# Optimization experiments

Measured on AMD Instinct MI355X. Metric: run time of the kernel, lower is better.

## Reference

```python
import jax, jax.numpy as jnp
import numpy as np
from jax import lax

SOS = -1
BLANK = 28
MAX_SYMBOLS = 4
T, B, ENC = 128, 32, 1024
VOCAB = 29   # includes blank at index 28
EMB = 320
HID = 320


def setup_inputs() -> dict:
    key = jax.random.key(0)
    ks = jax.random.split(key, 9)
    s = 0.1
    return {
        "x": jax.random.normal(ks[0], (T, B, ENC), jnp.float32),
        "lengths": jax.random.randint(ks[1], (B,), T // 2, T + 1, jnp.int32),
        "embedding": jax.random.normal(ks[2], (VOCAB - 1, EMB), jnp.float32) * s,
        "W_ih": jax.random.normal(ks[3], (4 * HID, EMB), jnp.float32) * s,
        "W_hh": jax.random.normal(ks[4], (4 * HID, HID), jnp.float32) * s,
        "b_ih": jax.random.normal(ks[5], (4 * HID,), jnp.float32) * s,
        "b_hh": jax.random.normal(ks[6], (4 * HID,), jnp.float32) * s,
        "W_joint": jax.random.normal(ks[7], (VOCAB, ENC + HID), jnp.float32) * s,
        "b_joint": jax.random.normal(ks[8], (VOCAB,), jnp.float32) * s,
    }


def _lstm_cell(xe, h, c, W_ih, W_hh, b_ih, b_hh):
    gates = xe @ W_ih.T + h @ W_hh.T + b_ih + b_hh          # [B, 4H]
    i, f, g, o = jnp.split(gates, 4, axis=-1)               # torch gate order
    i, f, o = jax.nn.sigmoid(i), jax.nn.sigmoid(f), jax.nn.sigmoid(o)
    g = jnp.tanh(g)
    c2 = f * c + i * g
    h2 = o * jnp.tanh(c2)
    return h2, c2


def _decode(x, lengths, embedding, W_ih, W_hh, b_ih, b_hh, W_joint, b_joint):
    Tn, Bn, _ = x.shape
    Lmax = Tn * MAX_SYMBOLS
    bidx = jnp.arange(Bn)

    def sym_step(carry, _):
        h, c, last, pos, labels, lps, active = carry
        # pred step: zero embedding for SOS, else embed (label>blank -> label-1)
        adj = jnp.where(last > BLANK, last - 1, last)
        adj = jnp.clip(adj, 0, VOCAB - 2)
        emb = jnp.where((last == SOS)[:, None], 0.0, embedding[adj])  # [B, EMB]
        h2, c2 = _lstm_cell(emb, h, c, W_ih, W_hh, b_ih, b_hh)
        # joint step: concat(enc frame, pred) -> fc -> log_softmax
        f_enc = carry_f                                            # closed over
        logits = jnp.concatenate([f_enc, h2], axis=-1) @ W_joint.T + b_joint
        logp = jax.nn.log_softmax(logits, axis=-1)                 # [B, V]
        idx = jnp.argmax(logp, axis=-1).astype(jnp.int32)
        v = jnp.take_along_axis(logp, idx[:, None].astype(jnp.int32), axis=-1)[:, 0]
        is_blank = idx == BLANK
        emit = active & (~is_blank)
        # commit hidden/label only on non-blank emission (as original)
        h = jnp.where(emit[:, None], h2, h)
        c = jnp.where(emit[:, None], c2, c)
        last = jnp.where(emit, idx, last)
        cur = labels[bidx, pos]
        labels = labels.at[bidx, pos].set(jnp.where(emit, idx, cur))
        lps = lps + jnp.where(active, v, 0.0)
        pos = pos + emit.astype(pos.dtype)
        active = active & (~is_blank)
        return (h, c, last, pos, labels, lps, active), None

    def time_step(carry, inp):
        f_t, t = inp                                              # f_t: [B, ENC]
        h, c, last, pos, labels, lps = carry
        active0 = t < lengths
        global carry_f
        carry_f = f_t
        (h, c, last, pos, labels, lps, _), _ = lax.scan(
            sym_step, (h, c, last, pos, labels, lps, active0), None,
            length=MAX_SYMBOLS)
        return (h, c, last, pos, labels, lps), None

    init = (
        jnp.zeros((Bn, HID), x.dtype),
        jnp.zeros((Bn, HID), x.dtype),
        jnp.full((Bn,), SOS, jnp.int32),
        jnp.zeros((Bn,), jnp.int32),
        jnp.full((Bn, Lmax), -1, jnp.int32),
        jnp.zeros((Bn,), x.dtype),
    )
    (h, c, last, pos, labels, lps), _ = lax.scan(
        time_step, init, (x, jnp.arange(Tn)))
    return labels, pos, lps


def reference(x, lengths, embedding, W_ih, W_hh, b_ih, b_hh, W_joint, b_joint):
    # labels: [B, T*MAX_SYMBOLS] int32, padded with -1
    # n_symbols: [B] number of emitted symbols per utterance
    # logp_sum: [B] sum of selected max log-probs over all evaluated decode steps
    labels, n_symbols, logp_sum = _decode(
        x, lengths, embedding, W_ih, W_hh, b_ih, b_hh, W_joint, b_joint)
    return labels, n_symbols, logp_sum
```

## Files before the change

### kernel.cpp

```cpp
#include <hip/hip_runtime.h>
#include <math.h>

typedef unsigned long long u64;
typedef unsigned int u32;

#define BN 32
#define TN 128
#define ENCD 1024
#define HID 320
#define NG 1280
#define VN 29
#define BLANKI 28
#define SLICES 8
#define UPS 40
#define ROWS 160
#define JW 1344
#define JSTR 41
#define XSTRIDE 70
#define NPOLL (7*69)

#define E_OFF   0
#define E_SZ    (TN*BN*VN)
#define P_OFF   (E_OFF + E_SZ)
#define P_SZ    (VN*NG)
#define X_OFF   (P_OFF + P_SZ)
#define X_U64S  (2*BN*SLICES*XSTRIDE)

__device__ __forceinline__ float dot4(float4 a, float4 b) {
    return a.x*b.x + a.y*b.y + a.z*b.z + a.w*b.w;
}
__device__ __forceinline__ u64 aload(const u64* p) {
    return __hip_atomic_load(p, __ATOMIC_RELAXED, __HIP_MEMORY_SCOPE_AGENT);
}
__device__ __forceinline__ void astore(u64* p, u64 v) {
    __hip_atomic_store(p, v, __ATOMIC_RELAXED, __HIP_MEMORY_SCOPE_AGENT);
}

__global__ __launch_bounds__(256) void k_enc(const float* __restrict__ x,
        const float* __restrict__ Wj, const float* __restrict__ bj,
        float* __restrict__ E, u64* __restrict__ xchg)
{
    __shared__ float xl[4][1056];
    const int tid = threadIdx.x;
    const int blk = blockIdx.x;
    const int t = blk >> 3, b0 = (blk & 7) * 4;

    if (tid < 35) xchg[(size_t)blk*35 + tid] = 0ull;

    #pragma unroll
    for (int bb = 0; bb < 4; ++bb) {
        const float4* src = (const float4*)(x + ((size_t)(t*BN + b0 + bb))*ENCD);
        float4 v4 = src[tid];
        ((float4*)&xl[bb][0])[tid + (tid >> 5)] = v4;
    }
    __syncthreads();
    if (tid < 232) {
        const int v = tid >> 3, k8 = tid & 7;
        float a0=0.f, a1=0.f, a2=0.f, a3=0.f;
        const float4* wrow = (const float4*)(Wj + (size_t)v*JW) + k8*32;
        const float4* x0 = ((const float4*)&xl[0][0]) + k8*33;
        const float4* x1 = ((const float4*)&xl[1][0]) + k8*33;
        const float4* x2 = ((const float4*)&xl[2][0]) + k8*33;
        const float4* x3 = ((const float4*)&xl[3][0]) + k8*33;
        #pragma unroll 4
        for (int m = 0; m < 32; ++m) {
            float4 w4 = wrow[m];
            a0 += dot4(w4, x0[m]);
            a1 += dot4(w4, x1[m]);
            a2 += dot4(w4, x2[m]);
            a3 += dot4(w4, x3[m]);
        }
        #pragma unroll
        for (int d = 1; d < 8; d <<= 1) {
            a0 += __shfl_xor(a0, d); a1 += __shfl_xor(a1, d);
            a2 += __shfl_xor(a2, d); a3 += __shfl_xor(a3, d);
        }
        if (k8 == 0) {
            float bjv = bj[v];
            E[((size_t)(t*BN + b0+0))*VN + v] = a0 + bjv;
            E[((size_t)(t*BN + b0+1))*VN + v] = a1 + bjv;
            E[((size_t)(t*BN + b0+2))*VN + v] = a2 + bjv;
            E[((size_t)(t*BN + b0+3))*VN + v] = a3 + bjv;
        }
    }
}

__global__ __launch_bounds__(256) void k_pred(const float* __restrict__ emb,
        const float* __restrict__ Wih, const float* __restrict__ bih,
        const float* __restrict__ bhh, float* __restrict__ P)
{
    __shared__ float el[HID];
    const int tid = threadIdx.x, j = blockIdx.x;
    if (tid < 80) {
        float4 v4 = make_float4(0.f, 0.f, 0.f, 0.f);
        if (j < 28) v4 = ((const float4*)(emb + (size_t)j*HID))[tid];
        ((float4*)el)[tid] = v4;
    }
    __syncthreads();
    #pragma unroll
    for (int q = 0; q < 5; ++q) {
        const int r = q*256 + tid;
        float acc = bih[r] + bhh[r];
        const float4* wrow = (const float4*)(Wih + (size_t)r*HID);
        #pragma unroll 8
        for (int k4 = 0; k4 < 80; ++k4)
            acc += dot4(wrow[k4], ((const float4*)el)[k4]);
        P[(size_t)j*NG + r] = acc;
    }
}

__global__ __launch_bounds__(256, 1) void k_dec(const int* __restrict__ lengths,
        const float* __restrict__ Whh, const float* __restrict__ Wj,
        const float* __restrict__ E, const float* __restrict__ P,
        u64* __restrict__ xchg, float* __restrict__ out)
{
    __shared__ float P_lds[VN*ROWS];
    __shared__ float Wjh[VN*JSTR];
    __shared__ float h2st[HID];
    __shared__ float c2st[UPS];
    __shared__ float gates[ROWS];
    __shared__ float plog_l[SLICES*VN];
    __shared__ float pad_force[14400];

    const int tid = threadIdx.x;
    const int bid = blockIdx.x;
    const int b = bid & 31, slice = bid >> 5;
    const int rg = tid >> 3, kg = tid & 7;
    const int lane = tid & 63;

    int len = lengths[b];
    if (len > TN) len = TN;
    if (len < 0) {
        pad_force[tid] = (float)tid;
        gates[tid & 127] = pad_force[(tid*7) & 14399];
    }

    float4 wq[50];
    #pragma unroll
    for (int q = 0; q < 5; ++q) {
        const int r = rg*5 + q;
        const int gt = r / 40, u = r - gt*40;
        const float4* wrow = (const float4*)(Whh + ((size_t)(gt*HID + slice*UPS + u))*HID + kg*40);
        #pragma unroll
        for (int jb = 0; jb < 10; ++jb) wq[q*10 + jb] = wrow[jb];
    }
    for (int i = tid; i < VN*ROWS; i += 256) {
        const int jj = i / ROWS, r = i - jj*ROWS;
        const int gt = r / 40, u = r - gt*40;
        P_lds[i] = P[(size_t)jj*NG + gt*HID + slice*UPS + u];
    }
    for (int i = tid; i < VN*UPS; i += 256) {
        const int v = i / UPS, k = i - v*UPS;
        Wjh[v*JSTR + k] = Wj[(size_t)v*JW + ENCD + slice*UPS + k];
    }
    if (tid < UPS) c2st[tid] = 0.f;
    if (slice == 0) for (int i = tid; i < 512; i += 256) out[b*512 + i] = -1.0f;
    __syncthreads();

    float lps = 0.f;
    float acc[5] = {0.f, 0.f, 0.f, 0.f, 0.f};
    float lsum_r = 0.f;
    int pos = 0, jrow = 28, n = 1;
    bool dirty = true;

    const int pw1 = tid;
    const bool has2 = (tid < NPOLL - 256);

    for (int t = 0; t < len; ++t) {
        const float Ereg = (lane < VN)
            ? E[((size_t)(t*BN + b))*VN + lane] : -INFINITY;

        for (int s = 0; s < 4; ++s) {
            if (dirty) {
                const int par = n & 1;
                const size_t mybase = ((size_t)(par*BN + b)*SLICES + slice)*XSTRIDE;
                if (kg == 0) {
                    #pragma unroll
                    for (int q = 0; q < 5; ++q) {
                        const int r = rg*5 + q;
                        gates[r] = acc[q] + P_lds[jrow*ROWS + r];
                    }
                }
                __syncthreads();
                if (tid < 64) {
                    if (tid < UPS) {
                        const float gi = gates[tid],      gf = gates[40+tid];
                        const float gg = gates[80+tid],   go = gates[120+tid];
                        const float ii = 1.f/(1.f+expf(-gi));
                        const float ff = 1.f/(1.f+expf(-gf));
                        const float oo = 1.f/(1.f+expf(-go));
                        const float G  = tanhf(gg);
                        const float c2 = ff*c2st[tid] + ii*G;
                        c2st[tid] = c2;
                        const float h2 = oo * tanhf(c2);
                        h2st[slice*UPS + tid] = h2;
                        const u64 pk = ((u64)(u32)n << 32) | (u64)__float_as_uint(h2);
                        astore(&xchg[mybase + tid], pk);
                    }
                    if (tid < VN) {
                        float pkv[8];
                        #pragma unroll
                        for (int k8 = 0; k8 < 8; ++k8) {
                            float pk = 0.f;
                            #pragma unroll
                            for (int m2 = 0; m2 < 5; ++m2)
                                pk += Wjh[tid*JSTR + k8*5 + m2]
                                    * h2st[slice*UPS + k8*5 + m2];
                            pkv[k8] = pk;
                        }
                        const float pp = ((pkv[0]+pkv[1])+(pkv[2]+pkv[3]))
                                       + ((pkv[4]+pkv[5])+(pkv[6]+pkv[7]));
                        plog_l[slice*VN + tid] = pp;
                        const u64 pk2 = ((u64)(u32)n << 32) | (u64)__float_as_uint(pp);
                        astore(&xchg[mybase + UPS + tid], pk2);
                    }
                }
                {
                    const size_t pbase = ((size_t)(par*BN + b)*SLICES)*XSTRIDE;
                    int j1 = pw1 / 69; const int w1 = pw1 - j1*69;
                    j1 += (j1 >= slice);
                    u64* p1 = (u64*)&xchg[pbase + (size_t)j1*XSTRIDE + w1];
                    bool need1 = true, need2 = has2;
                    int j2 = 0, w2 = 0; u64* p2 = p1;
                    if (has2) {
                        const int i2 = tid + 256;
                        j2 = i2 / 69; w2 = i2 - j2*69;
                        j2 += (j2 >= slice);
                        p2 = (u64*)&xchg[pbase + (size_t)j2*XSTRIDE + w2];
                    }
                    int cap = 0;
                    while ((need1 | need2) && cap < (1 << 16)) {
                        u64 v1 = 0, v2 = 0;
                        if (need1) v1 = aload(p1);
                        if (need2) v2 = aload(p2);
                        if (need1 && (u32)(v1 >> 32) == (u32)n) {
                            const float f = __uint_as_float((u32)v1);
                            if (w1 < UPS) h2st[j1*UPS + w1] = f;
                            else          plog_l[j1*VN + (w1 - UPS)] = f;
                            need1 = false;
                        }
                        if (need2 && (u32)(v2 >> 32) == (u32)n) {
                            const float f = __uint_as_float((u32)v2);
                            if (w2 < UPS) h2st[j2*UPS + w2] = f;
                            else          plog_l[j2*VN + (w2 - UPS)] = f;
                            need2 = false;
                        }
                        ++cap;
                    }
                }
                __syncthreads();
                {
                    float a2[5] = {0.f, 0.f, 0.f, 0.f, 0.f};
                    #pragma unroll
                    for (int jb = 0; jb < 10; ++jb) {
                        float4 hv = *(const float4*)(h2st + kg*40 + jb*4);
                        #pragma unroll
                        for (int q = 0; q < 5; ++q) a2[q] += dot4(wq[q*10 + jb], hv);
                    }
                    #pragma unroll
                    for (int q = 0; q < 5; ++q) {
                        a2[q] += __shfl_xor(a2[q], 1);
                        a2[q] += __shfl_xor(a2[q], 2);
                        a2[q] += __shfl_xor(a2[q], 4);
                        acc[q] = a2[q];
                    }
                }
                if (lane < VN) {
                    float sA = 0.f;
                    #pragma unroll
                    for (int j2 = 0; j2 < SLICES; ++j2) sA += plog_l[j2*VN + lane];
                    lsum_r = sA;
                }
                n++;
            }
            const float Lv = (lane < VN) ? (Ereg + lsum_r) : -INFINITY;
            float m = Lv; int ai = lane;
            #pragma unroll
            for (int d = 1; d < 64; d <<= 1) {
                const float om = __shfl_xor(m, d);
                const int   oi = __shfl_xor(ai, d);
                if (om > m || (om == m && oi < ai)) { m = om; ai = oi; }
            }
            float e = (lane < VN) ? expf(Lv - m) : 0.f;
            #pragma unroll
            for (int d = 1; d < 64; d <<= 1) e += __shfl_xor(e, d);
            lps += -logf(e);

            if (ai == BLANKI) { dirty = false; break; }
            if (slice == 0 && tid == 0) out[b*512 + pos] = (float)ai;
            pos++;
            jrow = ai;
            dirty = true;
        }
    }

    if (slice == 0 && tid == 0) {
        out[16384 + b] = (float)pos;
        out[16416 + b] = lps;
    }
}

extern "C" void kernel_launch(void* const* d_in, const int* in_sizes, int n_in,
                              void* d_out, int out_size, void* d_ws, size_t ws_size,
                              hipStream_t stream) {
    const float* x    = (const float*)d_in[0];
    const int* lens   = (const int*)  d_in[1];
    const float* emb  = (const float*)d_in[2];
    const float* Wih  = (const float*)d_in[3];
    const float* Whh  = (const float*)d_in[4];
    const float* bih  = (const float*)d_in[5];
    const float* bhh  = (const float*)d_in[6];
    const float* Wj   = (const float*)d_in[7];
    const float* bj   = (const float*)d_in[8];
    float* out = (float*)d_out;
    float* ws  = (float*)d_ws;

    float* E    = ws + E_OFF;
    float* P    = ws + P_OFF;
    u64*   xchg = (u64*)(ws + X_OFF);

    hipLaunchKernelGGL(k_enc,  dim3(1024), dim3(256), 0, stream, x, Wj, bj, E, xchg);
    hipLaunchKernelGGL(k_pred, dim3(29),   dim3(256), 0, stream, emb, Wih, bih, bhh, P);
    hipLaunchKernelGGL(k_dec,  dim3(256),  dim3(256), 0, stream,
                       lens, Whh, Wj, E, P, xchg, out);
}
```

Measured before the change: 1.643 ms.

## Compute full joint pred projection locally instead of exchanging partial logits

Each decoder block stops publishing per-slice partial joint logits through the global exchange buffer. It now polls only the hidden-state slices of the other blocks and computes the full hidden-to-vocab projection locally, with the weights held in registers. This shrinks the exchange record per slice and removes the 29-element logit work from the critical path before publishing. Polling moves to threads 64 and up so the gate-update wave is not blocked. In exchange, every block does redundant projection work, and an extra block barrier plus register pressure (40 more floats per thread) are added.

```diff
diff --git a/kernel.cpp b/kernel.cpp
--- a/kernel.cpp
+++ b/kernel.cpp
@@ -15,9 +15,8 @@
 #define UPS 40
 #define ROWS 160
 #define JW 1344
-#define JSTR 41
-#define XSTRIDE 70
-#define NPOLL (7*69)
+#define XSTRIDE 48
+#define NPOLL (7*UPS)
 
 #define E_OFF   0
 #define E_SZ    (TN*BN*VN)
@@ -45,7 +44,7 @@
     const int blk = blockIdx.x;
     const int t = blk >> 3, b0 = (blk & 7) * 4;
 
-    if (tid < 35) xchg[(size_t)blk*35 + tid] = 0ull;
+    if (tid < 24) xchg[(size_t)blk*24 + tid] = 0ull;
 
     #pragma unroll
     for (int bb = 0; bb < 4; ++bb) {
@@ -115,12 +114,11 @@
         u64* __restrict__ xchg, float* __restrict__ out)
 {
     __shared__ float P_lds[VN*ROWS];
-    __shared__ float Wjh[VN*JSTR];
     __shared__ float h2st[HID];
     __shared__ float c2st[UPS];
     __shared__ float gates[ROWS];
-    __shared__ float plog_l[SLICES*VN];
-    __shared__ float pad_force[14400];
+    __shared__ float lsum[32];
+    __shared__ float pad_force[15500];
 
     const int tid = threadIdx.x;
     const int bid = blockIdx.x;
@@ -132,7 +130,7 @@
     if (len > TN) len = TN;
     if (len < 0) {
         pad_force[tid] = (float)tid;
-        gates[tid & 127] = pad_force[(tid*7) & 14399];
+        gates[tid & 127] = pad_force[(tid*7) & 15499];
     }
 
     float4 wq[50];
@@ -149,9 +147,18 @@
         const int gt = r / 40, u = r - gt*40;
         P_lds[i] = P[(size_t)jj*NG + gt*HID + slice*UPS + u];
     }
-    for (int i = tid; i < VN*UPS; i += 256) {
-        const int v = i / UPS, k = i - v*UPS;
-        Wjh[v*JSTR + k] = Wj[(size_t)v*JW + ENCD + slice*UPS + k];
+    float wjr[40];
+    if (tid < 232) {
+        const int v = tid >> 3, k8 = tid & 7;
+        const float* wv = Wj + (size_t)v*JW + ENCD + k8*5;
+        #pragma unroll
+        for (int j2 = 0; j2 < 8; ++j2)
+            #pragma unroll
+            for (int m2 = 0; m2 < 5; ++m2)
+                wjr[j2*5 + m2] = wv[j2*40 + m2];
+    } else {
+        #pragma unroll
+        for (int i = 0; i < 40; ++i) wjr[i] = 0.f;
     }
     if (tid < UPS) c2st[tid] = 0.f;
     if (slice == 0) for (int i = tid; i < 512; i += 256) out[b*512 + i] = -1.0f;
@@ -163,8 +170,9 @@
     int pos = 0, jrow = 28, n = 1;
     bool dirty = true;
 
-    const int pw1 = tid;
-    const bool has2 = (tid < NPOLL - 256);
+    const int pw1 = tid - 64;
+    const bool isPoller = (pw1 >= 0);
+    const bool has2 = isPoller && (pw1 < NPOLL - 192);
 
     for (int t = 0; t < len; ++t) {
         const float Ereg = (lane < VN)
@@ -197,36 +205,18 @@
                         const u64 pk = ((u64)(u32)n << 32) | (u64)__float_as_uint(h2);
                         astore(&xchg[mybase + tid], pk);
                     }
-                    if (tid < VN) {
-                        float pkv[8];
-                        #pragma unroll
-                        for (int k8 = 0; k8 < 8; ++k8) {
-                            float pk = 0.f;
-                            #pragma unroll
-                            for (int m2 = 0; m2 < 5; ++m2)
-                                pk += Wjh[tid*JSTR + k8*5 + m2]
-                                    * h2st[slice*UPS + k8*5 + m2];
-                            pkv[k8] = pk;
-                        }
-                        const float pp = ((pkv[0]+pkv[1])+(pkv[2]+pkv[3]))
-                                       + ((pkv[4]+pkv[5])+(pkv[6]+pkv[7]));
-                        plog_l[slice*VN + tid] = pp;
-                        const u64 pk2 = ((u64)(u32)n << 32) | (u64)__float_as_uint(pp);
-                        astore(&xchg[mybase + UPS + tid], pk2);
-                    }
-                }
-                {
+                } else {
                     const size_t pbase = ((size_t)(par*BN + b)*SLICES)*XSTRIDE;
-                    int j1 = pw1 / 69; const int w1 = pw1 - j1*69;
+                    int j1 = pw1 / UPS; const int w1 = pw1 - j1*UPS;
                     j1 += (j1 >= slice);
-                    u64* p1 = (u64*)&xchg[pbase + (size_t)j1*XSTRIDE + w1];
+                    const u64* p1 = &xchg[pbase + (size_t)j1*XSTRIDE + w1];
                     bool need1 = true, need2 = has2;
-                    int j2 = 0, w2 = 0; u64* p2 = p1;
+                    int j2_ = 0, w2 = 0; const u64* p2 = p1;
                     if (has2) {
-                        const int i2 = tid + 256;
-                        j2 = i2 / 69; w2 = i2 - j2*69;
-                        j2 += (j2 >= slice);
-                        p2 = (u64*)&xchg[pbase + (size_t)j2*XSTRIDE + w2];
+                        const int i2 = pw1 + 192;
+                        j2_ = i2 / UPS; w2 = i2 - j2_*UPS;
+                        j2_ += (j2_ >= slice);
+                        p2 = &xchg[pbase + (size_t)j2_*XSTRIDE + w2];
                     }
                     int cap = 0;
                     while ((need1 | need2) && cap < (1 << 16)) {
@@ -234,21 +224,33 @@
                         if (need1) v1 = aload(p1);
                         if (need2) v2 = aload(p2);
                         if (need1 && (u32)(v1 >> 32) == (u32)n) {
-                            const float f = __uint_as_float((u32)v1);
-                            if (w1 < UPS) h2st[j1*UPS + w1] = f;
-                            else          plog_l[j1*VN + (w1 - UPS)] = f;
+                            h2st[j1*UPS + w1] = __uint_as_float((u32)v1);
                             need1 = false;
                         }
                         if (need2 && (u32)(v2 >> 32) == (u32)n) {
-                            const float f = __uint_as_float((u32)v2);
-                            if (w2 < UPS) h2st[j2*UPS + w2] = f;
-                            else          plog_l[j2*VN + (w2 - UPS)] = f;
+                            h2st[j2_*UPS + w2] = __uint_as_float((u32)v2);
                             need2 = false;
                         }
                         ++cap;
                     }
                 }
                 __syncthreads();
+                if (tid < 232) {
+                    const int v = tid >> 3, k8 = tid & 7;
+                    float sA = 0.f;
+                    #pragma unroll
+                    for (int j2 = 0; j2 < 8; ++j2) {
+                        float pk = 0.f;
+                        #pragma unroll
+                        for (int m2 = 0; m2 < 5; ++m2)
+                            pk += wjr[j2*5 + m2] * h2st[j2*UPS + k8*5 + m2];
+                        pk += __shfl_xor(pk, 1);
+                        pk += __shfl_xor(pk, 2);
+                        pk += __shfl_xor(pk, 4);
+                        sA += pk;
+                    }
+                    if (k8 == 0) lsum[v] = sA;
+                }
                 {
                     float a2[5] = {0.f, 0.f, 0.f, 0.f, 0.f};
                     #pragma unroll
@@ -265,12 +267,8 @@
                         acc[q] = a2[q];
                     }
                 }
-                if (lane < VN) {
-                    float sA = 0.f;
-                    #pragma unroll
-                    for (int j2 = 0; j2 < SLICES; ++j2) sA += plog_l[j2*VN + lane];
-                    lsum_r = sA;
-                }
+                __syncthreads();
+                lsum_r = (lane < VN) ? lsum[lane] : 0.f;
                 n++;
             }
             const float Lv = (lane < VN) ? (Ereg + lsum_r) : -INFINITY;
```

Result: slower. 1.824 ms (+11.0%).

## Use L2-local plain stores and nt loads for cross-block exchange when co-located on one XCC

Applied to the files above, without the earlier changes.

Each decoder block reads its XCC ID, and the eight slice blocks of a batch element check whether they all sit on the same XCC, followed by a token handshake that tests plain-store visibility. If every check passes, the per-step h2 and partial-logit exchange uses plain global stores and non-temporal loads instead of agent-scope atomics. The aim is lower exchange latency through the shared L2 on the recurrent critical path. In exchange there is extra startup handshaking, a larger zeroed xchg region, and reliance on hardware coherence behaviour that holds only when the blocks share an XCC; otherwise the code falls back to the atomic path.

```diff
diff --git a/kernel.cpp b/kernel.cpp
--- a/kernel.cpp
+++ b/kernel.cpp
@@ -25,6 +25,10 @@
 #define P_SZ    (VN*NG)
 #define X_OFF   (P_OFF + P_SZ)
 #define X_U64S  (2*BN*SLICES*XSTRIDE)
+#define TOK_OFF X_U64S
+#define HS_OFF  (TOK_OFF + BN*SLICES*16)
+#define OK_OFF  (HS_OFF + BN*SLICES)
+#define TOTAL_U64S (OK_OFF + BN*SLICES)
 
 __device__ __forceinline__ float dot4(float4 a, float4 b) {
     return a.x*b.x + a.y*b.y + a.z*b.z + a.w*b.w;
@@ -34,6 +38,21 @@
 }
 __device__ __forceinline__ void astore(u64* p, u64 v) {
     __hip_atomic_store(p, v, __ATOMIC_RELAXED, __HIP_MEMORY_SCOPE_AGENT);
+}
+__device__ __forceinline__ void pstore(u64* p, u64 v) {
+    asm volatile("global_store_dwordx2 %0, %1, off" :: "v"(p), "v"(v) : "memory");
+}
+__device__ __forceinline__ u64 ntload(const u64* p) {
+    u64 r;
+    asm volatile("global_load_dwordx2 %0, %1, off nt\n\ts_waitcnt vmcnt(0)"
+                 : "=v"(r) : "v"(p) : "memory");
+    return r;
+}
+__device__ __forceinline__ void xstore(u64* p, u64 v, bool fast) {
+    if (fast) pstore(p, v); else astore(p, v);
+}
+__device__ __forceinline__ u64 xload(const u64* p, bool fast) {
+    return fast ? ntload(p) : aload(p);
 }
 
 __global__ __launch_bounds__(256) void k_enc(const float* __restrict__ x,
@@ -45,7 +64,10 @@
     const int blk = blockIdx.x;
     const int t = blk >> 3, b0 = (blk & 7) * 4;
 
-    if (tid < 35) xchg[(size_t)blk*35 + tid] = 0ull;
+    if (tid < 40) {
+        const int idx = blk*40 + tid;
+        if (idx < TOTAL_U64S) xchg[idx] = 0ull;
+    }
 
     #pragma unroll
     for (int bb = 0; bb < 4; ++bb) {
@@ -120,7 +142,9 @@
     __shared__ float c2st[UPS];
     __shared__ float gates[ROWS];
     __shared__ float plog_l[SLICES*VN];
-    __shared__ float pad_force[14400];
+    __shared__ int   xccok, flag_fast;
+    __shared__ int   okv1[8], okv2[8];
+    __shared__ float pad_force[14300];
 
     const int tid = threadIdx.x;
     const int bid = blockIdx.x;
@@ -128,11 +152,17 @@
     const int rg = tid >> 3, kg = tid & 7;
     const int lane = tid & 63;
 
+    if (tid == 0) {
+        u32 xcc;
+        asm volatile("s_getreg_b32 %0, hwreg(HW_REG_XCC_ID)" : "=s"(xcc));
+        astore(&xchg[HS_OFF + b*SLICES + slice], (u64)(xcc & 0xFFu) | 0x100ull);
+    }
+
     int len = lengths[b];
     if (len > TN) len = TN;
     if (len < 0) {
         pad_force[tid] = (float)tid;
-        gates[tid & 127] = pad_force[(tid*7) & 14399];
+        gates[tid & 127] = pad_force[(tid*7) & 14299];
     }
 
     float4 wq[50];
@@ -155,7 +185,55 @@
     }
     if (tid < UPS) c2st[tid] = 0.f;
     if (slice == 0) for (int i = tid; i < 512; i += 256) out[b*512 + i] = -1.0f;
-    __syncthreads();
+    if (tid < 8) { okv1[tid] = 1; okv2[tid] = 1; }
+
+    if (tid == 0) {
+        bool ok = true; u32 x0 = 0;
+        for (int j = 0; j < SLICES; ++j) {
+            u64 v = 0; int cap = 0;
+            do { v = aload(&xchg[HS_OFF + b*SLICES + j]); }
+            while (!(v & 0x100ull) && ++cap < (1 << 22));
+            if (!(v & 0x100ull)) { ok = false; break; }
+            const u32 xv = (u32)(v & 0xFFu);
+            if (xv >= 8u) { ok = false; break; }
+            if (j == 0) x0 = xv; else if (xv != x0) { ok = false; break; }
+        }
+        xccok = ok ? 1 : 0;
+    }
+    __syncthreads();
+
+    u64* mytok = &xchg[TOK_OFF + (size_t)(b*SLICES + slice)*16];
+    if (tid == 0) pstore(mytok, 1ull);
+    if (tid < 8 && tid != slice && xccok) {
+        const u64* pt = &xchg[TOK_OFF + (size_t)(b*SLICES + tid)*16];
+        u64 v = 0; int cap = 0;
+        do { v = ntload(pt); } while (v < 1ull && ++cap < (1 << 12));
+        if (v < 1ull) okv1[tid] = 0;
+    }
+    __syncthreads();
+    if (tid == 0) pstore(mytok, 2ull);
+    if (tid < 8 && tid != slice && xccok) {
+        const u64* pt = &xchg[TOK_OFF + (size_t)(b*SLICES + tid)*16];
+        u64 v = 0; int cap = 0;
+        do { v = ntload(pt); } while (v < 2ull && ++cap < (1 << 12));
+        if (v < 2ull) okv2[tid] = 0;
+    }
+    __syncthreads();
+    if (tid == 0) {
+        bool ok = (xccok != 0);
+        for (int j = 0; j < 8; ++j) ok = ok && okv1[j] && okv2[j];
+        astore(&xchg[OK_OFF + b*SLICES + slice], ok ? 3ull : 2ull);
+        bool allok = true;
+        for (int j = 0; j < SLICES; ++j) {
+            u64 v = 0; int cap = 0;
+            do { v = aload(&xchg[OK_OFF + b*SLICES + j]); }
+            while (v < 2ull && ++cap < (1 << 22));
+            if (v != 3ull) allok = false;
+        }
+        flag_fast = allok ? 1 : 0;
+    }
+    __syncthreads();
+    const bool fast = (flag_fast != 0);
 
     float lps = 0.f;
     float acc[5] = {0.f, 0.f, 0.f, 0.f, 0.f};
@@ -195,7 +273,7 @@
                         const float h2 = oo * tanhf(c2);
                         h2st[slice*UPS + tid] = h2;
                         const u64 pk = ((u64)(u32)n << 32) | (u64)__float_as_uint(h2);
-                        astore(&xchg[mybase + tid], pk);
+                        xstore(&xchg[mybase + tid], pk, fast);
                     }
                     if (tid < VN) {
                         float pkv[8];
@@ -212,7 +290,7 @@
                                        + ((pkv[4]+pkv[5])+(pkv[6]+pkv[7]));
                         plog_l[slice*VN + tid] = pp;
                         const u64 pk2 = ((u64)(u32)n << 32) | (u64)__float_as_uint(pp);
-                        astore(&xchg[mybase + UPS + tid], pk2);
+                        xstore(&xchg[mybase + UPS + tid], pk2, fast);
                     }
                 }
                 {
@@ -231,8 +309,8 @@
                     int cap = 0;
                     while ((need1 | need2) && cap < (1 << 16)) {
                         u64 v1 = 0, v2 = 0;
-                        if (need1) v1 = aload(p1);
-                        if (need2) v2 = aload(p2);
+                        if (need1) v1 = xload(p1, fast);
+                        if (need2) v2 = xload(p2, fast);
                         if (need1 && (u32)(v1 >> 32) == (u32)n) {
                             const float f = __uint_as_float((u32)v1);
                             if (w1 < UPS) h2st[j1*UPS + w1] = f;
```

New measurement: 1.808 ms. 1.1x slower.
